# Performance work log

Hardware: AMD Instinct MI355X
Metric: run time of the kernel (lower is better)

## Reference

```python
import jax, jax.numpy as jnp
import numpy as np

N_USERS = 100000
N_ITEMS = 50000
N_NODES = N_USERS + N_ITEMS
EMB_DIM = 128
N_LAYERS = 3
NNZ = 2400000
MASK_PROB = 0.2


def setup_inputs() -> dict:
    key = jax.random.key(0)
    ks = jax.random.split(key, 8)
    user_emb = jax.random.normal(ks[0], (N_USERS, EMB_DIM), dtype=jnp.float32) * 0.1
    item_emb = jax.random.normal(ks[1], (N_ITEMS, EMB_DIM), dtype=jnp.float32) * 0.1
    adj_rows = jax.random.randint(ks[2], (NNZ,), 0, N_NODES, dtype=jnp.int32)
    adj_cols = jax.random.randint(ks[3], (NNZ,), 0, N_NODES, dtype=jnp.int32)
    # stand-in for symmetric-normalized adjacency values
    adj_vals = jax.random.uniform(ks[4], (NNZ,), dtype=jnp.float32) * (1.0 / 16.0)
    # deterministic version of mask_embeddings' random binary mask
    mask = (jax.random.uniform(ks[5], (N_USERS, EMB_DIM)) > MASK_PROB).astype(jnp.float32)
    # Dense(emb_dim, relu) params (Glorot-like scale)
    attr_w = jax.random.normal(ks[6], (EMB_DIM, EMB_DIM), dtype=jnp.float32) * (1.0 / np.sqrt(EMB_DIM))
    attr_b = jnp.zeros((EMB_DIM,), dtype=jnp.float32)
    return {"user_emb": user_emb, "item_emb": item_emb, "adj_rows": adj_rows,
            "adj_cols": adj_cols, "adj_vals": adj_vals, "mask": mask,
            "attr_w": attr_w, "attr_b": attr_b}


def _spmm(rows, cols, vals, x):
    # sparse [N,N] @ dense [N,d] via gather + segment_sum
    return jax.ops.segment_sum(vals[:, None] * x[cols], rows, num_segments=N_NODES)


def reference(user_emb, item_emb, adj_rows, adj_cols, adj_vals, mask, attr_w, attr_b):
    alpha = 1.0 / (N_LAYERS + 1)
    all_emb = jnp.concatenate([user_emb, item_emb], axis=0)  # [N, d]
    combined = alpha * all_emb
    for _ in range(N_LAYERS):
        all_emb = _spmm(adj_rows, adj_cols, adj_vals, all_emb)
        combined = combined + alpha * all_emb
    user_final = combined[:N_USERS]
    item_final = combined[N_USERS:]
    masked_user_emb = user_final * mask
    predicted_attributes = jax.nn.relu(masked_user_emb @ attr_w + attr_b)
    return (user_final, item_final, masked_user_emb, predicted_attributes, mask)
```

## Files before the change

### kernel.cpp

```cpp
#include <hip/hip_runtime.h>

#define N_USERS 100000
#define N_ITEMS 50000
#define N_NODES 150000
#define NNZ     2400000
#define ALPHA   0.25f
#define VSCALE  262144.0f
#define VINV    (1.0f / 262144.0f)

static __device__ __forceinline__ unsigned int f2bf(float f) {
    unsigned int u = __float_as_uint(f);
    u += 0x7fffu + ((u >> 16) & 1u);
    return u >> 16;
}
static __device__ __forceinline__ float bflo(unsigned int w) { return __uint_as_float(w << 16); }
static __device__ __forceinline__ float bfhi(unsigned int w) { return __uint_as_float(w & 0xffff0000u); }

static __device__ __forceinline__ int xcd_swz(int orig, int q, int rem) {
    int xcd = orig & 7, idx = orig >> 3;
    return (xcd < rem ? xcd * (q + 1) : rem * (q + 1) + (xcd - rem) * q) + idx;
}

__global__ void k_init(const float4* __restrict__ ue, const float4* __restrict__ ie,
                       uint4* __restrict__ x0) {
    int i = blockIdx.x * 256 + threadIdx.x;
    if (i >= N_NODES * 16) return;
    float4 a, b;
    if (i < N_USERS * 16) { a = ue[2 * i]; b = ue[2 * i + 1]; }
    else { int k = i - N_USERS * 16; a = ie[2 * k]; b = ie[2 * k + 1]; }
    uint4 o;
    o.x = f2bf(a.x) | (f2bf(a.y) << 16);
    o.y = f2bf(a.z) | (f2bf(a.w) << 16);
    o.z = f2bf(b.x) | (f2bf(b.y) << 16);
    o.w = f2bf(b.z) | (f2bf(b.w) << 16);
    x0[i] = o;
}

__global__ void k_histrank(const int* __restrict__ rows, int* __restrict__ cnt,
                           int* __restrict__ rank) {
    int stride = gridDim.x * blockDim.x;
    for (int i = blockIdx.x * blockDim.x + threadIdx.x; i < NNZ; i += stride)
        rank[i] = atomicAdd(&cnt[rows[i]], 1);
}

__global__ void k_scan1(const int* __restrict__ cnt, int* __restrict__ tmp, int* __restrict__ part) {
    __shared__ int sm[1024];
    int g = blockIdx.x * 1024 + threadIdx.x;
    int v = (g < N_NODES) ? cnt[g] : 0;
    sm[threadIdx.x] = v;
    __syncthreads();
    for (int off = 1; off < 1024; off <<= 1) {
        int t = (threadIdx.x >= off) ? sm[threadIdx.x - off] : 0;
        __syncthreads();
        sm[threadIdx.x] += t;
        __syncthreads();
    }
    if (g < N_NODES) tmp[g] = sm[threadIdx.x];
    if (threadIdx.x == 1023) part[blockIdx.x] = sm[1023];
}

__global__ void k_scan2(int* __restrict__ part, int n) {
    __shared__ int sm[256];
    int v = (threadIdx.x < n) ? part[threadIdx.x] : 0;
    sm[threadIdx.x] = v;
    __syncthreads();
    for (int off = 1; off < 256; off <<= 1) {
        int t = (threadIdx.x >= off) ? sm[threadIdx.x - off] : 0;
        __syncthreads();
        sm[threadIdx.x] += t;
        __syncthreads();
    }
    if (threadIdx.x < n) part[threadIdx.x] = sm[threadIdx.x];
}

__global__ void k_scan3(const int* __restrict__ tmp, const int* __restrict__ part, int* __restrict__ rp) {
    int g = blockIdx.x * 1024 + threadIdx.x;
    if (g < N_NODES) {
        int add = blockIdx.x ? part[blockIdx.x - 1] : 0;
        rp[g + 1] = tmp[g] + add;
    }
    if (g == 0) rp[0] = 0;
}

__launch_bounds__(256)
__global__ void k_scatter(const int* __restrict__ rows, const int* __restrict__ cols,
                          const float* __restrict__ vals, const int* __restrict__ rank,
                          const int* __restrict__ rp, unsigned int* __restrict__ ev) {
    int cls = blockIdx.x & 7;
    int base = (blockIdx.x >> 3) * 256 + threadIdx.x;
    for (int i = base; i < NNZ; i += 65536) {
        int r = rows[i];
        if (((r >> 11) & 7) != cls) continue;
        int v14 = (int)(vals[i] * VSCALE + 0.5f);
        v14 = min(v14, 16383);
        unsigned int w = ((unsigned int)cols[i] << 14) | (unsigned int)v14;
        ev[rp[r] + rank[i]] = w;
    }
}

__launch_bounds__(256)
__global__ void k_spmm(const int* __restrict__ rp, const unsigned int* __restrict__ ev,
                       const unsigned short* __restrict__ x, unsigned short* __restrict__ y) {
    int b = xcd_swz(blockIdx.x, 4687, 4);
    int r = b * 4 + __builtin_amdgcn_readfirstlane(threadIdx.x >> 6);
    if (r >= N_NODES) return;
    int l = (threadIdx.x & 63) * 2;
    const unsigned short* xp = x + l;
    float ax = 0.f, ay = 0.f;
    int s = rp[r], e = rp[r + 1];
    int j = s;
    for (; j + 4 <= e; j += 4) {
        unsigned int m0 = ev[j], m1 = ev[j + 1], m2 = ev[j + 2], m3 = ev[j + 3];
        unsigned int w0 = *(const unsigned int*)(xp + (m0 >> 14) * 128);
        unsigned int w1 = *(const unsigned int*)(xp + (m1 >> 14) * 128);
        unsigned int w2 = *(const unsigned int*)(xp + (m2 >> 14) * 128);
        unsigned int w3 = *(const unsigned int*)(xp + (m3 >> 14) * 128);
        float v0 = (m0 & 16383u) * VINV, v1 = (m1 & 16383u) * VINV;
        float v2 = (m2 & 16383u) * VINV, v3 = (m3 & 16383u) * VINV;
        ax += v0 * bflo(w0) + v1 * bflo(w1) + v2 * bflo(w2) + v3 * bflo(w3);
        ay += v0 * bfhi(w0) + v1 * bfhi(w1) + v2 * bfhi(w2) + v3 * bfhi(w3);
    }
    for (; j < e; ++j) {
        unsigned int m = ev[j];
        unsigned int w = *(const unsigned int*)(xp + (m >> 14) * 128);
        float v = (m & 16383u) * VINV;
        ax += v * bflo(w);
        ay += v * bfhi(w);
    }
    unsigned int o = f2bf(ax) | (f2bf(ay) << 16);
    *(unsigned int*)(y + r * 128 + l) = o;
}

__launch_bounds__(256)
__global__ void k_spmm3(const int* __restrict__ rp, const unsigned int* __restrict__ ev,
                        const unsigned short* __restrict__ y2src,
                        const unsigned short* __restrict__ y1,
                        const float2* __restrict__ ue2, const float2* __restrict__ ie2,
                        const float2* __restrict__ mask2,
                        float2* __restrict__ comb2, float2* __restrict__ masked2,
                        float2* __restrict__ maskO2) {
    int b = xcd_swz(blockIdx.x, 4687, 4);
    int r = b * 4 + __builtin_amdgcn_readfirstlane(threadIdx.x >> 6);
    if (r >= N_NODES) return;
    int l = threadIdx.x & 63;
    const unsigned short* xp = y2src + 2 * l;
    float ax = 0.f, ay = 0.f;
    int s = rp[r], e = rp[r + 1];
    int j = s;
    for (; j + 4 <= e; j += 4) {
        unsigned int m0 = ev[j], m1 = ev[j + 1], m2 = ev[j + 2], m3 = ev[j + 3];
        unsigned int w0 = *(const unsigned int*)(xp + (m0 >> 14) * 128);
        unsigned int w1 = *(const unsigned int*)(xp + (m1 >> 14) * 128);
        unsigned int w2 = *(const unsigned int*)(xp + (m2 >> 14) * 128);
        unsigned int w3 = *(const unsigned int*)(xp + (m3 >> 14) * 128);
        float v0 = (m0 & 16383u) * VINV, v1 = (m1 & 16383u) * VINV;
        float v2 = (m2 & 16383u) * VINV, v3 = (m3 & 16383u) * VINV;
        ax += v0 * bflo(w0) + v1 * bflo(w1) + v2 * bflo(w2) + v3 * bflo(w3);
        ay += v0 * bfhi(w0) + v1 * bfhi(w1) + v2 * bfhi(w2) + v3 * bfhi(w3);
    }
    for (; j < e; ++j) {
        unsigned int m = ev[j];
        unsigned int w = *(const unsigned int*)(xp + (m >> 14) * 128);
        float v = (m & 16383u) * VINV;
        ax += v * bflo(w);
        ay += v * bfhi(w);
    }
    float2 em = (r < N_USERS) ? ue2[r * 64 + l] : ie2[(r - N_USERS) * 64 + l];
    unsigned int a1 = *(const unsigned int*)(y1    + r * 128 + 2 * l);
    unsigned int a2 = *(const unsigned int*)(y2src + r * 128 + 2 * l);
    float cx = ALPHA * (em.x + bflo(a1) + bflo(a2) + ax);
    float cy = ALPHA * (em.y + bfhi(a1) + bfhi(a2) + ay);
    comb2[r * 64 + l] = make_float2(cx, cy);
    if (r < N_USERS) {
        float2 m = mask2[r * 64 + l];
        masked2[r * 64 + l] = make_float2(cx * m.x, cy * m.y);
        maskO2[r * 64 + l]  = m;
    }
}

__launch_bounds__(256)
__global__ void k_mm(const float* __restrict__ A, const float* __restrict__ W,
                     const float* __restrict__ b, float* __restrict__ pred) {
    __shared__ float Wl[128 * 128];
    float4* W4s = (float4*)Wl;
    const float4* W4g = (const float4*)W;
    for (int i = threadIdx.x; i < 4096; i += 256) W4s[i] = W4g[i];
    __syncthreads();

    int rowt = threadIdx.x >> 3;
    int colg = threadIdx.x & 7;
    int row  = blockIdx.x * 32 + rowt;
    const float* ar = A + row * 128;

    float4 a0 = make_float4(0, 0, 0, 0), a1 = a0, a2 = a0, a3 = a0;
    for (int k = 0; k < 128; ++k) {
        float av = ar[k];
        float4 w0 = W4s[k * 32 + colg];
        float4 w1 = W4s[k * 32 + colg + 8];
        float4 w2 = W4s[k * 32 + colg + 16];
        float4 w3 = W4s[k * 32 + colg + 24];
        a0.x += av * w0.x; a0.y += av * w0.y; a0.z += av * w0.z; a0.w += av * w0.w;
        a1.x += av * w1.x; a1.y += av * w1.y; a1.z += av * w1.z; a1.w += av * w1.w;
        a2.x += av * w2.x; a2.y += av * w2.y; a2.z += av * w2.z; a2.w += av * w2.w;
        a3.x += av * w3.x; a3.y += av * w3.y; a3.z += av * w3.z; a3.w += av * w3.w;
    }
    const float4* b4 = (const float4*)b;
    float4* out4 = (float4*)pred;
    float4 acc[4] = {a0, a1, a2, a3};
    #pragma unroll
    for (int jj = 0; jj < 4; ++jj) {
        float4 bb = b4[colg + 8 * jj];
        float4 r;
        r.x = fmaxf(acc[jj].x + bb.x, 0.f);
        r.y = fmaxf(acc[jj].y + bb.y, 0.f);
        r.z = fmaxf(acc[jj].z + bb.z, 0.f);
        r.w = fmaxf(acc[jj].w + bb.w, 0.f);
        out4[row * 32 + colg + 8 * jj] = r;
    }
}

extern "C" void kernel_launch(void* const* d_in, const int* in_sizes, int n_in,
                              void* d_out, int out_size, void* d_ws, size_t ws_size,
                              hipStream_t stream) {
    const float* ue     = (const float*)d_in[0];
    const float* ie     = (const float*)d_in[1];
    const int*   arows  = (const int*)d_in[2];
    const int*   acols  = (const int*)d_in[3];
    const float* avals  = (const float*)d_in[4];
    const float* mask   = (const float*)d_in[5];
    const float* attr_w = (const float*)d_in[6];
    const float* attr_b = (const float*)d_in[7];
    float* out = (float*)d_out;

    float* comb   = out;
    float* masked = out + 19200000;
    float* pred   = out + 32000000;
    float* maskO  = out + 44800000;

    char* ws = (char*)d_ws;
    unsigned short* x0b  = (unsigned short*)(ws);
    unsigned short* y1   = (unsigned short*)(ws +  38400000);
    unsigned short* y2   = (unsigned short*)(ws +  76800000);
    int*            rank = (int*)          (ws + 115200000);
    unsigned int*   ev   = (unsigned int*) (ws + 124800000);
    int*            cnt  = (int*)          (ws + 134400000);
    int*            rp   = (int*)          (ws + 135000064);
    int*            tmp  = (int*)          (ws + 135600128);
    int*            part = (int*)          (ws + 136200192);

    hipMemsetAsync(cnt, 0, (N_NODES + 1) * sizeof(int), stream);
    k_init<<<9375, 256, 0, stream>>>((const float4*)ue, (const float4*)ie, (uint4*)x0b);
    k_histrank<<<2048, 256, 0, stream>>>(arows, cnt, rank);
    k_scan1<<<147, 1024, 0, stream>>>(cnt, tmp, part);
    k_scan2<<<1, 256, 0, stream>>>(part, 147);
    k_scan3<<<147, 1024, 0, stream>>>(tmp, part, rp);
    k_scatter<<<2048, 256, 0, stream>>>(arows, acols, avals, rank, rp, ev);

    k_spmm<<<37500, 256, 0, stream>>>(rp, ev, x0b, y1);
    k_spmm<<<37500, 256, 0, stream>>>(rp, ev, y1, y2);
    k_spmm3<<<37500, 256, 0, stream>>>(rp, ev, y2, y1,
                                       (const float2*)ue, (const float2*)ie,
                                       (const float2*)mask,
                                       (float2*)comb, (float2*)masked, (float2*)maskO);

    k_mm<<<3125, 256, 0, stream>>>(masked, attr_w, attr_b, pred);
}
```

Baseline: 886.3 us.

## Two-pass bucketed CSR build via row-range staging and unroll SpMM gather by 8

Replaces the histogram-rank plus filtered scatter CSR build with a chunked partition pass that stages packed (row,val)/(col,val) records into 8 row-range buckets, then runs the histogram and an atomic-cursor placement per bucket, so atomics and writes stay localized and the scatter no longer rereads all of NNZ eight times. The SpMM kernels also gain an 8-wide unrolled gather loop to keep more loads in flight. This adds a staging buffer and extra atomics on the cursor array, and within-row edge order becomes nondeterministic, which can change float summation order.

Result: slower. 927.7 us (+4.7%).

```diff
diff --git a/kernel.cpp b/kernel.cpp
--- a/kernel.cpp
+++ b/kernel.cpp
@@ -7,6 +7,9 @@
 #define ALPHA   0.25f
 #define VSCALE  262144.0f
 #define VINV    (1.0f / 262144.0f)
+#define CHUNK   4096
+#define NCHUNK  ((NNZ + CHUNK - 1) / CHUNK)
+#define CAPC    327680
 
 static __device__ __forceinline__ unsigned int f2bf(float f) {
     unsigned int u = __float_as_uint(f);
@@ -36,11 +39,62 @@
     x0[i] = o;
 }
 
-__global__ void k_histrank(const int* __restrict__ rows, int* __restrict__ cnt,
-                           int* __restrict__ rank) {
-    int stride = gridDim.x * blockDim.x;
-    for (int i = blockIdx.x * blockDim.x + threadIdx.x; i < NNZ; i += stride)
-        rank[i] = atomicAdd(&cnt[rows[i]], 1);
+__launch_bounds__(256)
+__global__ void k_part(const int* __restrict__ rows, const int* __restrict__ cols,
+                       const float* __restrict__ vals, uint2* __restrict__ stg,
+                       int* __restrict__ clsCur) {
+    __shared__ int hcnt[8], hoff[8], gbase[8];
+    __shared__ uint2 buf[CHUNK];
+    int cid = blockIdx.x;
+    int base = cid * CHUNK;
+    int e = min(CHUNK, NNZ - base);
+    if (threadIdx.x < 8) hcnt[threadIdx.x] = 0;
+    __syncthreads();
+
+    uint2 myrec[16];
+    int   mypos[16];
+    int   cnt_i = 0;
+    for (int i = threadIdx.x; i < e; i += 256) {
+        int r = rows[base + i];
+        int c = cols[base + i];
+        float v = vals[base + i];
+        int v14 = min((int)(v * VSCALE + 0.5f), 16383);
+        int cls = r / 18750;
+        int lr = atomicAdd(&hcnt[cls], 1);
+        myrec[cnt_i] = make_uint2(((unsigned)r << 14) | (unsigned)v14,
+                                  ((unsigned)c << 14) | (unsigned)v14);
+        mypos[cnt_i] = (lr << 3) | cls;
+        ++cnt_i;
+    }
+    __syncthreads();
+    if (threadIdx.x == 0) {
+        int s = 0;
+        for (int k = 0; k < 8; ++k) { hoff[k] = s; s += hcnt[k]; }
+    }
+    __syncthreads();
+    if (threadIdx.x < 8 && hcnt[threadIdx.x] > 0)
+        gbase[threadIdx.x] = atomicAdd(&clsCur[threadIdx.x], hcnt[threadIdx.x]);
+    __syncthreads();
+    for (int k = 0; k < cnt_i; ++k)
+        buf[hoff[mypos[k] & 7] + (mypos[k] >> 3)] = myrec[k];
+    __syncthreads();
+    for (int c8 = 0; c8 < 8; ++c8) {
+        int n = hcnt[c8], off = hoff[c8], gb = gbase[c8];
+        for (int i = threadIdx.x; i < n; i += 256)
+            stg[(size_t)c8 * CAPC + gb + i] = buf[off + i];
+    }
+}
+
+__launch_bounds__(256)
+__global__ void k_histB(const uint2* __restrict__ stg, const int* __restrict__ clsCur,
+                        int* __restrict__ cnt) {
+    int cls = blockIdx.x & 7;
+    int n = clsCur[cls];
+    const uint2* s = stg + (size_t)cls * CAPC;
+    int tid = (blockIdx.x >> 3) * 256 + threadIdx.x;
+    int stride = (gridDim.x >> 3) * 256;
+    for (int i = tid; i < n; i += stride)
+        atomicAdd(&cnt[s[i].x >> 14], 1);
 }
 
 __global__ void k_scan1(const int* __restrict__ cnt, int* __restrict__ tmp, int* __restrict__ part) {
@@ -73,28 +127,30 @@
     if (threadIdx.x < n) part[threadIdx.x] = sm[threadIdx.x];
 }
 
-__global__ void k_scan3(const int* __restrict__ tmp, const int* __restrict__ part, int* __restrict__ rp) {
+__global__ void k_scan3(const int* __restrict__ tmp, const int* __restrict__ part,
+                        int* __restrict__ rp, int* __restrict__ cursor) {
     int g = blockIdx.x * 1024 + threadIdx.x;
     if (g < N_NODES) {
         int add = blockIdx.x ? part[blockIdx.x - 1] : 0;
-        rp[g + 1] = tmp[g] + add;
-    }
-    if (g == 0) rp[0] = 0;
-}
-
-__launch_bounds__(256)
-__global__ void k_scatter(const int* __restrict__ rows, const int* __restrict__ cols,
-                          const float* __restrict__ vals, const int* __restrict__ rank,
-                          const int* __restrict__ rp, unsigned int* __restrict__ ev) {
+        int v = tmp[g] + add;
+        rp[g + 1] = v;
+        cursor[g + 1] = v;
+    }
+    if (g == 0) { rp[0] = 0; cursor[0] = 0; }
+}
+
+__launch_bounds__(256)
+__global__ void k_placeB(const uint2* __restrict__ stg, const int* __restrict__ clsCur,
+                         int* __restrict__ cursor, unsigned int* __restrict__ ev) {
     int cls = blockIdx.x & 7;
-    int base = (blockIdx.x >> 3) * 256 + threadIdx.x;
-    for (int i = base; i < NNZ; i += 65536) {
-        int r = rows[i];
-        if (((r >> 11) & 7) != cls) continue;
-        int v14 = (int)(vals[i] * VSCALE + 0.5f);
-        v14 = min(v14, 16383);
-        unsigned int w = ((unsigned int)cols[i] << 14) | (unsigned int)v14;
-        ev[rp[r] + rank[i]] = w;
+    int n = clsCur[cls];
+    const uint2* s = stg + (size_t)cls * CAPC;
+    int tid = (blockIdx.x >> 3) * 256 + threadIdx.x;
+    int stride = (gridDim.x >> 3) * 256;
+    for (int i = tid; i < n; i += stride) {
+        uint2 rec = s[i];
+        int p = atomicAdd(&cursor[rec.x >> 14], 1);
+        ev[p] = rec.y;
     }
 }
 
@@ -109,6 +165,26 @@
     float ax = 0.f, ay = 0.f;
     int s = rp[r], e = rp[r + 1];
     int j = s;
+    for (; j + 8 <= e; j += 8) {
+        unsigned int m0 = ev[j],     m1 = ev[j + 1], m2 = ev[j + 2], m3 = ev[j + 3];
+        unsigned int m4 = ev[j + 4], m5 = ev[j + 5], m6 = ev[j + 6], m7 = ev[j + 7];
+        unsigned int w0 = *(const unsigned int*)(xp + (m0 >> 14) * 128);
+        unsigned int w1 = *(const unsigned int*)(xp + (m1 >> 14) * 128);
+        unsigned int w2 = *(const unsigned int*)(xp + (m2 >> 14) * 128);
+        unsigned int w3 = *(const unsigned int*)(xp + (m3 >> 14) * 128);
+        unsigned int w4 = *(const unsigned int*)(xp + (m4 >> 14) * 128);
+        unsigned int w5 = *(const unsigned int*)(xp + (m5 >> 14) * 128);
+        unsigned int w6 = *(const unsigned int*)(xp + (m6 >> 14) * 128);
+        unsigned int w7 = *(const unsigned int*)(xp + (m7 >> 14) * 128);
+        float v0 = (m0 & 16383u) * VINV, v1 = (m1 & 16383u) * VINV;
+        float v2 = (m2 & 16383u) * VINV, v3 = (m3 & 16383u) * VINV;
+        float v4 = (m4 & 16383u) * VINV, v5 = (m5 & 16383u) * VINV;
+        float v6 = (m6 & 16383u) * VINV, v7 = (m7 & 16383u) * VINV;
+        ax += v0 * bflo(w0) + v1 * bflo(w1) + v2 * bflo(w2) + v3 * bflo(w3);
+        ay += v0 * bfhi(w0) + v1 * bfhi(w1) + v2 * bfhi(w2) + v3 * bfhi(w3);
+        ax += v4 * bflo(w4) + v5 * bflo(w5) + v6 * bflo(w6) + v7 * bflo(w7);
+        ay += v4 * bfhi(w4) + v5 * bfhi(w5) + v6 * bfhi(w6) + v7 * bfhi(w7);
+    }
     for (; j + 4 <= e; j += 4) {
         unsigned int m0 = ev[j], m1 = ev[j + 1], m2 = ev[j + 2], m3 = ev[j + 3];
         unsigned int w0 = *(const unsigned int*)(xp + (m0 >> 14) * 128);
@@ -147,6 +223,26 @@
     float ax = 0.f, ay = 0.f;
     int s = rp[r], e = rp[r + 1];
     int j = s;
+    for (; j + 8 <= e; j += 8) {
+        unsigned int m0 = ev[j],     m1 = ev[j + 1], m2 = ev[j + 2], m3 = ev[j + 3];
+        unsigned int m4 = ev[j + 4], m5 = ev[j + 5], m6 = ev[j + 6], m7 = ev[j + 7];
+        unsigned int w0 = *(const unsigned int*)(xp + (m0 >> 14) * 128);
+        unsigned int w1 = *(const unsigned int*)(xp + (m1 >> 14) * 128);
+        unsigned int w2 = *(const unsigned int*)(xp + (m2 >> 14) * 128);
+        unsigned int w3 = *(const unsigned int*)(xp + (m3 >> 14) * 128);
+        unsigned int w4 = *(const unsigned int*)(xp + (m4 >> 14) * 128);
+        unsigned int w5 = *(const unsigned int*)(xp + (m5 >> 14) * 128);
+        unsigned int w6 = *(const unsigned int*)(xp + (m6 >> 14) * 128);
+        unsigned int w7 = *(const unsigned int*)(xp + (m7 >> 14) * 128);
+        float v0 = (m0 & 16383u) * VINV, v1 = (m1 & 16383u) * VINV;
+        float v2 = (m2 & 16383u) * VINV, v3 = (m3 & 16383u) * VINV;
+        float v4 = (m4 & 16383u) * VINV, v5 = (m5 & 16383u) * VINV;
+        float v6 = (m6 & 16383u) * VINV, v7 = (m7 & 16383u) * VINV;
+        ax += v0 * bflo(w0) + v1 * bflo(w1) + v2 * bflo(w2) + v3 * bflo(w3);
+        ay += v0 * bfhi(w0) + v1 * bfhi(w1) + v2 * bfhi(w2) + v3 * bfhi(w3);
+        ax += v4 * bflo(w4) + v5 * bflo(w5) + v6 * bflo(w6) + v7 * bflo(w7);
+        ay += v4 * bfhi(w4) + v5 * bfhi(w5) + v6 * bfhi(w6) + v7 * bfhi(w7);
+    }
     for (; j + 4 <= e; j += 4) {
         unsigned int m0 = ev[j], m1 = ev[j + 1], m2 = ev[j + 2], m3 = ev[j + 3];
         unsigned int w0 = *(const unsigned int*)(xp + (m0 >> 14) * 128);
@@ -238,23 +334,26 @@
     float* maskO  = out + 44800000;
 
     char* ws = (char*)d_ws;
-    unsigned short* x0b  = (unsigned short*)(ws);
-    unsigned short* y1   = (unsigned short*)(ws +  38400000);
-    unsigned short* y2   = (unsigned short*)(ws +  76800000);
-    int*            rank = (int*)          (ws + 115200000);
-    unsigned int*   ev   = (unsigned int*) (ws + 124800000);
-    int*            cnt  = (int*)          (ws + 134400000);
-    int*            rp   = (int*)          (ws + 135000064);
-    int*            tmp  = (int*)          (ws + 135600128);
-    int*            part = (int*)          (ws + 136200192);
-
-    hipMemsetAsync(cnt, 0, (N_NODES + 1) * sizeof(int), stream);
+    unsigned short* x0b    = (unsigned short*)(ws);
+    unsigned short* y1     = (unsigned short*)(ws +  38400000);
+    unsigned short* y2     = (unsigned short*)(ws +  76800000);
+    uint2*          stg    = (uint2*)        (ws + 115200000);
+    unsigned int*   ev     = (unsigned int*) (ws + 136171520);
+    int*            cnt    = (int*)          (ws + 145771520);
+    int*            clsCur = (int*)          (ws + 146371584);
+    int*            rp     = (int*)          (ws + 146371648);
+    int*            cursor = (int*)          (ws + 146971712);
+    int*            tmp    = (int*)          (ws + 147571776);
+    int*            part   = (int*)          (ws + 148171840);
+
+    hipMemsetAsync(cnt, 0, 600064 + 64, stream);
     k_init<<<9375, 256, 0, stream>>>((const float4*)ue, (const float4*)ie, (uint4*)x0b);
-    k_histrank<<<2048, 256, 0, stream>>>(arows, cnt, rank);
+    k_part<<<NCHUNK, 256, 0, stream>>>(arows, acols, avals, stg, clsCur);
+    k_histB<<<2048, 256, 0, stream>>>(stg, clsCur, cnt);
     k_scan1<<<147, 1024, 0, stream>>>(cnt, tmp, part);
     k_scan2<<<1, 256, 0, stream>>>(part, 147);
-    k_scan3<<<147, 1024, 0, stream>>>(tmp, part, rp);
-    k_scatter<<<2048, 256, 0, stream>>>(arows, acols, avals, rank, rp, ev);
+    k_scan3<<<147, 1024, 0, stream>>>(tmp, part, rp, cursor);
+    k_placeB<<<2048, 256, 0, stream>>>(stg, clsCur, cursor, ev);
 
     k_spmm<<<37500, 256, 0, stream>>>(rp, ev, x0b, y1);
     k_spmm<<<37500, 256, 0, stream>>>(rp, ev, y1, y2);
```

## Quantize intermediate embeddings to per-row int8 for SpMM gathers

Applied to the files above, without the earlier changes.

Replaces the bf16 intermediate node embeddings with int8 values plus a per-row float scale, computed by a wave-wide max reduction. The SpMM kernels gather 2-byte lane words instead of 4-byte ones, halving gather traffic, and fold the row scale into the edge weight. The cost is a max-reduction per row, an extra scale load per edge, and a large loss of precision that may break accuracy tolerance.

After: 878.6 us. No clear change (-0.9%).

```diff
diff --git a/kernel.cpp b/kernel.cpp
--- a/kernel.cpp
+++ b/kernel.cpp
@@ -8,32 +8,37 @@
 #define VSCALE  262144.0f
 #define VINV    (1.0f / 262144.0f)
 
-static __device__ __forceinline__ unsigned int f2bf(float f) {
-    unsigned int u = __float_as_uint(f);
-    u += 0x7fffu + ((u >> 16) & 1u);
-    return u >> 16;
-}
-static __device__ __forceinline__ float bflo(unsigned int w) { return __uint_as_float(w << 16); }
-static __device__ __forceinline__ float bfhi(unsigned int w) { return __uint_as_float(w & 0xffff0000u); }
-
 static __device__ __forceinline__ int xcd_swz(int orig, int q, int rem) {
     int xcd = orig & 7, idx = orig >> 3;
     return (xcd < rem ? xcd * (q + 1) : rem * (q + 1) + (xcd - rem) * q) + idx;
 }
 
-__global__ void k_init(const float4* __restrict__ ue, const float4* __restrict__ ie,
-                       uint4* __restrict__ x0) {
-    int i = blockIdx.x * 256 + threadIdx.x;
-    if (i >= N_NODES * 16) return;
-    float4 a, b;
-    if (i < N_USERS * 16) { a = ue[2 * i]; b = ue[2 * i + 1]; }
-    else { int k = i - N_USERS * 16; a = ie[2 * k]; b = ie[2 * k + 1]; }
-    uint4 o;
-    o.x = f2bf(a.x) | (f2bf(a.y) << 16);
-    o.y = f2bf(a.z) | (f2bf(a.w) << 16);
-    o.z = f2bf(b.x) | (f2bf(b.y) << 16);
-    o.w = f2bf(b.z) | (f2bf(b.w) << 16);
-    x0[i] = o;
+static __device__ __forceinline__ float wave_max64(float m) {
+    #pragma unroll
+    for (int off = 32; off >= 1; off >>= 1)
+        m = fmaxf(m, __shfl_xor(m, off, 64));
+    return m;
+}
+
+static __device__ __forceinline__ float i8lo(unsigned short w) {
+    return (float)(signed char)(w & 0xff);
+}
+static __device__ __forceinline__ float i8hi(unsigned short w) {
+    return (float)(signed char)(w >> 8);
+}
+
+__launch_bounds__(256)
+__global__ void k_initq(const float2* __restrict__ ue2, const float2* __restrict__ ie2,
+                        unsigned short* __restrict__ xq, float* __restrict__ scl) {
+    int r = blockIdx.x * 4 + __builtin_amdgcn_readfirstlane(threadIdx.x >> 6);
+    if (r >= N_NODES) return;
+    int l = threadIdx.x & 63;
+    float2 v = (r < N_USERS) ? ue2[r * 64 + l] : ie2[(r - N_USERS) * 64 + l];
+    float m = wave_max64(fmaxf(fabsf(v.x), fabsf(v.y)));
+    float inv = (m > 0.f) ? 127.0f / m : 0.f;
+    int q0 = (int)rintf(v.x * inv), q1 = (int)rintf(v.y * inv);
+    xq[r * 64 + l] = (unsigned short)((q0 & 0xff) | ((q1 & 0xff) << 8));
+    if (l == 0) scl[r] = m * (1.0f / 127.0f);
 }
 
 __global__ void k_histrank(const int* __restrict__ rows, int* __restrict__ cnt,
@@ -99,77 +104,94 @@
 }
 
 __launch_bounds__(256)
-__global__ void k_spmm(const int* __restrict__ rp, const unsigned int* __restrict__ ev,
-                       const unsigned short* __restrict__ x, unsigned short* __restrict__ y) {
+__global__ void k_spmmq(const int* __restrict__ rp, const unsigned int* __restrict__ ev,
+                        const unsigned short* __restrict__ xq, const float* __restrict__ sclx,
+                        unsigned short* __restrict__ yq, float* __restrict__ scly) {
     int b = xcd_swz(blockIdx.x, 4687, 4);
     int r = b * 4 + __builtin_amdgcn_readfirstlane(threadIdx.x >> 6);
     if (r >= N_NODES) return;
-    int l = (threadIdx.x & 63) * 2;
-    const unsigned short* xp = x + l;
+    int l = threadIdx.x & 63;
     float ax = 0.f, ay = 0.f;
     int s = rp[r], e = rp[r + 1];
     int j = s;
     for (; j + 4 <= e; j += 4) {
         unsigned int m0 = ev[j], m1 = ev[j + 1], m2 = ev[j + 2], m3 = ev[j + 3];
-        unsigned int w0 = *(const unsigned int*)(xp + (m0 >> 14) * 128);
-        unsigned int w1 = *(const unsigned int*)(xp + (m1 >> 14) * 128);
-        unsigned int w2 = *(const unsigned int*)(xp + (m2 >> 14) * 128);
-        unsigned int w3 = *(const unsigned int*)(xp + (m3 >> 14) * 128);
-        float v0 = (m0 & 16383u) * VINV, v1 = (m1 & 16383u) * VINV;
-        float v2 = (m2 & 16383u) * VINV, v3 = (m3 & 16383u) * VINV;
-        ax += v0 * bflo(w0) + v1 * bflo(w1) + v2 * bflo(w2) + v3 * bflo(w3);
-        ay += v0 * bfhi(w0) + v1 * bfhi(w1) + v2 * bfhi(w2) + v3 * bfhi(w3);
+        int c0 = __builtin_amdgcn_readfirstlane((int)(m0 >> 14));
+        int c1 = __builtin_amdgcn_readfirstlane((int)(m1 >> 14));
+        int c2 = __builtin_amdgcn_readfirstlane((int)(m2 >> 14));
+        int c3 = __builtin_amdgcn_readfirstlane((int)(m3 >> 14));
+        unsigned short w0 = xq[c0 * 64 + l];
+        unsigned short w1 = xq[c1 * 64 + l];
+        unsigned short w2 = xq[c2 * 64 + l];
+        unsigned short w3 = xq[c3 * 64 + l];
+        float f0 = (float)(m0 & 16383u) * VINV * sclx[c0];
+        float f1 = (float)(m1 & 16383u) * VINV * sclx[c1];
+        float f2 = (float)(m2 & 16383u) * VINV * sclx[c2];
+        float f3 = (float)(m3 & 16383u) * VINV * sclx[c3];
+        ax += f0 * i8lo(w0) + f1 * i8lo(w1) + f2 * i8lo(w2) + f3 * i8lo(w3);
+        ay += f0 * i8hi(w0) + f1 * i8hi(w1) + f2 * i8hi(w2) + f3 * i8hi(w3);
     }
     for (; j < e; ++j) {
         unsigned int m = ev[j];
-        unsigned int w = *(const unsigned int*)(xp + (m >> 14) * 128);
-        float v = (m & 16383u) * VINV;
-        ax += v * bflo(w);
-        ay += v * bfhi(w);
-    }
-    unsigned int o = f2bf(ax) | (f2bf(ay) << 16);
-    *(unsigned int*)(y + r * 128 + l) = o;
-}
-
-__launch_bounds__(256)
-__global__ void k_spmm3(const int* __restrict__ rp, const unsigned int* __restrict__ ev,
-                        const unsigned short* __restrict__ y2src,
-                        const unsigned short* __restrict__ y1,
-                        const float2* __restrict__ ue2, const float2* __restrict__ ie2,
-                        const float2* __restrict__ mask2,
-                        float2* __restrict__ comb2, float2* __restrict__ masked2,
-                        float2* __restrict__ maskO2) {
+        int c = __builtin_amdgcn_readfirstlane((int)(m >> 14));
+        unsigned short w = xq[c * 64 + l];
+        float f = (float)(m & 16383u) * VINV * sclx[c];
+        ax += f * i8lo(w);
+        ay += f * i8hi(w);
+    }
+    float m = wave_max64(fmaxf(fabsf(ax), fabsf(ay)));
+    float inv = (m > 0.f) ? 127.0f / m : 0.f;
+    int q0 = (int)rintf(ax * inv), q1 = (int)rintf(ay * inv);
+    yq[r * 64 + l] = (unsigned short)((q0 & 0xff) | ((q1 & 0xff) << 8));
+    if (l == 0) scly[r] = m * (1.0f / 127.0f);
+}
+
+__launch_bounds__(256)
+__global__ void k_spmm3q(const int* __restrict__ rp, const unsigned int* __restrict__ ev,
+                         const unsigned short* __restrict__ y2q, const float* __restrict__ scl2,
+                         const unsigned short* __restrict__ y1q, const float* __restrict__ scl1,
+                         const float2* __restrict__ ue2, const float2* __restrict__ ie2,
+                         const float2* __restrict__ mask2,
+                         float2* __restrict__ comb2, float2* __restrict__ masked2,
+                         float2* __restrict__ maskO2) {
     int b = xcd_swz(blockIdx.x, 4687, 4);
     int r = b * 4 + __builtin_amdgcn_readfirstlane(threadIdx.x >> 6);
     if (r >= N_NODES) return;
     int l = threadIdx.x & 63;
-    const unsigned short* xp = y2src + 2 * l;
     float ax = 0.f, ay = 0.f;
     int s = rp[r], e = rp[r + 1];
     int j = s;
     for (; j + 4 <= e; j += 4) {
         unsigned int m0 = ev[j], m1 = ev[j + 1], m2 = ev[j + 2], m3 = ev[j + 3];
-        unsigned int w0 = *(const unsigned int*)(xp + (m0 >> 14) * 128);
-        unsigned int w1 = *(const unsigned int*)(xp + (m1 >> 14) * 128);
-        unsigned int w2 = *(const unsigned int*)(xp + (m2 >> 14) * 128);
-        unsigned int w3 = *(const unsigned int*)(xp + (m3 >> 14) * 128);
-        float v0 = (m0 & 16383u) * VINV, v1 = (m1 & 16383u) * VINV;
-        float v2 = (m2 & 16383u) * VINV, v3 = (m3 & 16383u) * VINV;
-        ax += v0 * bflo(w0) + v1 * bflo(w1) + v2 * bflo(w2) + v3 * bflo(w3);
-        ay += v0 * bfhi(w0) + v1 * bfhi(w1) + v2 * bfhi(w2) + v3 * bfhi(w3);
+        int c0 = __builtin_amdgcn_readfirstlane((int)(m0 >> 14));
+        int c1 = __builtin_amdgcn_readfirstlane((int)(m1 >> 14));
+        int c2 = __builtin_amdgcn_readfirstlane((int)(m2 >> 14));
+        int c3 = __builtin_amdgcn_readfirstlane((int)(m3 >> 14));
+        unsigned short w0 = y2q[c0 * 64 + l];
+        unsigned short w1 = y2q[c1 * 64 + l];
+        unsigned short w2 = y2q[c2 * 64 + l];
+        unsigned short w3 = y2q[c3 * 64 + l];
+        float f0 = (float)(m0 & 16383u) * VINV * scl2[c0];
+        float f1 = (float)(m1 & 16383u) * VINV * scl2[c1];
+        float f2 = (float)(m2 & 16383u) * VINV * scl2[c2];
+        float f3 = (float)(m3 & 16383u) * VINV * scl2[c3];
+        ax += f0 * i8lo(w0) + f1 * i8lo(w1) + f2 * i8lo(w2) + f3 * i8lo(w3);
+        ay += f0 * i8hi(w0) + f1 * i8hi(w1) + f2 * i8hi(w2) + f3 * i8hi(w3);
     }
     for (; j < e; ++j) {
         unsigned int m = ev[j];
-        unsigned int w = *(const unsigned int*)(xp + (m >> 14) * 128);
-        float v = (m & 16383u) * VINV;
-        ax += v * bflo(w);
-        ay += v * bfhi(w);
+        int c = __builtin_amdgcn_readfirstlane((int)(m >> 14));
+        unsigned short w = y2q[c * 64 + l];
+        float f = (float)(m & 16383u) * VINV * scl2[c];
+        ax += f * i8lo(w);
+        ay += f * i8hi(w);
     }
     float2 em = (r < N_USERS) ? ue2[r * 64 + l] : ie2[(r - N_USERS) * 64 + l];
-    unsigned int a1 = *(const unsigned int*)(y1    + r * 128 + 2 * l);
-    unsigned int a2 = *(const unsigned int*)(y2src + r * 128 + 2 * l);
-    float cx = ALPHA * (em.x + bflo(a1) + bflo(a2) + ax);
-    float cy = ALPHA * (em.y + bfhi(a1) + bfhi(a2) + ay);
+    float s1 = scl1[r], s2 = scl2[r];
+    unsigned short a1 = y1q[r * 64 + l];
+    unsigned short a2 = y2q[r * 64 + l];
+    float cx = ALPHA * (em.x + s1 * i8lo(a1) + s2 * i8lo(a2) + ax);
+    float cy = ALPHA * (em.y + s1 * i8hi(a1) + s2 * i8hi(a2) + ay);
     comb2[r * 64 + l] = make_float2(cx, cy);
     if (r < N_USERS) {
         float2 m = mask2[r * 64 + l];
@@ -238,30 +260,33 @@
     float* maskO  = out + 44800000;
 
     char* ws = (char*)d_ws;
-    unsigned short* x0b  = (unsigned short*)(ws);
-    unsigned short* y1   = (unsigned short*)(ws +  38400000);
-    unsigned short* y2   = (unsigned short*)(ws +  76800000);
-    int*            rank = (int*)          (ws + 115200000);
-    unsigned int*   ev   = (unsigned int*) (ws + 124800000);
-    int*            cnt  = (int*)          (ws + 134400000);
-    int*            rp   = (int*)          (ws + 135000064);
-    int*            tmp  = (int*)          (ws + 135600128);
-    int*            part = (int*)          (ws + 136200192);
+    unsigned short* x0q  = (unsigned short*)(ws);
+    unsigned short* y1q  = (unsigned short*)(ws + 19200000);
+    unsigned short* y2q  = (unsigned short*)(ws + 38400000);
+    float*          scl0 = (float*)        (ws + 57600000);
+    float*          scl1 = (float*)        (ws + 58200000);
+    float*          scl2 = (float*)        (ws + 58800000);
+    int*            rank = (int*)          (ws + 59400000);
+    unsigned int*   ev   = (unsigned int*) (ws + 69000000);
+    int*            cnt  = (int*)          (ws + 78600000);
+    int*            rp   = (int*)          (ws + 79200064);
+    int*            tmp  = (int*)          (ws + 79800128);
+    int*            part = (int*)          (ws + 80400192);
 
     hipMemsetAsync(cnt, 0, (N_NODES + 1) * sizeof(int), stream);
-    k_init<<<9375, 256, 0, stream>>>((const float4*)ue, (const float4*)ie, (uint4*)x0b);
+    k_initq<<<37500, 256, 0, stream>>>((const float2*)ue, (const float2*)ie, x0q, scl0);
     k_histrank<<<2048, 256, 0, stream>>>(arows, cnt, rank);
     k_scan1<<<147, 1024, 0, stream>>>(cnt, tmp, part);
     k_scan2<<<1, 256, 0, stream>>>(part, 147);
     k_scan3<<<147, 1024, 0, stream>>>(tmp, part, rp);
     k_scatter<<<2048, 256, 0, stream>>>(arows, acols, avals, rank, rp, ev);
 
-    k_spmm<<<37500, 256, 0, stream>>>(rp, ev, x0b, y1);
-    k_spmm<<<37500, 256, 0, stream>>>(rp, ev, y1, y2);
-    k_spmm3<<<37500, 256, 0, stream>>>(rp, ev, y2, y1,
-                                       (const float2*)ue, (const float2*)ie,
-                                       (const float2*)mask,
-                                       (float2*)comb, (float2*)masked, (float2*)maskO);
+    k_spmmq<<<37500, 256, 0, stream>>>(rp, ev, x0q, scl0, y1q, scl1);
+    k_spmmq<<<37500, 256, 0, stream>>>(rp, ev, y1q, scl1, y2q, scl2);
+    k_spmm3q<<<37500, 256, 0, stream>>>(rp, ev, y2q, scl2, y1q, scl1,
+                                        (const float2*)ue, (const float2*)ie,
+                                        (const float2*)mask,
+                                        (float2*)comb, (float2*)masked, (float2*)maskO);
 
     k_mm<<<3125, 256, 0, stream>>>(masked, attr_w, attr_b, pred);
 }
```
